# Performance work log

Measured on AMD Instinct MI355X. Metric: run time of the kernel, lower is better.

## Reference

```python
import jax, jax.numpy as jnp
import numpy as np

OBS_DIM = 256
ACTION_DIM = 4
NUM_OBJECTS = 16
HIDDEN = 512
BATCH = 4096
LN_EPS = 1e-5


def _uniform(key, shape, stdv):
    return jax.random.uniform(key, shape, jnp.float32, -stdv, stdv)


def setup_inputs() -> dict:
    key = jax.random.key(0)
    ks = jax.random.split(key, 8)
    node_in = OBS_DIM + ACTION_DIM
    s1 = 1.0 / np.sqrt(HIDDEN)
    s3 = 1.0 / np.sqrt(OBS_DIM)
    return {
        "states": jax.random.normal(ks[0], (BATCH, NUM_OBJECTS, OBS_DIM), jnp.float32),
        "action": jax.random.randint(ks[1], (BATCH,), 0, ACTION_DIM * NUM_OBJECTS, jnp.int64 if jax.config.jax_enable_x64 else jnp.int32),
        "W1": _uniform(ks[2], (node_in, HIDDEN), s1),
        "b1": _uniform(ks[3], (HIDDEN,), s1),
        "W2": _uniform(ks[4], (HIDDEN, HIDDEN), s1),
        "b2": _uniform(ks[5], (HIDDEN,), s1),
        "W3": _uniform(ks[6], (HIDDEN, OBS_DIM), s3),
        "b3": _uniform(ks[7], (OBS_DIM,), s3),
        "ln_g": jnp.ones((HIDDEN,), jnp.float32),
        "ln_b": jnp.zeros((HIDDEN,), jnp.float32),
    }


def _gc(x, W, b):
    # x: [B, O, d_in]. adj = block_diag(ones(O,O)/O) == per-graph mean pooling,
    # broadcast back to every node in the graph.
    s = jnp.einsum("bod,dh->boh", x, W)
    m = jnp.mean(s, axis=1, keepdims=True)  # [B, 1, h]
    return jnp.broadcast_to(m, s.shape) + b


def _layernorm(x, g, b):
    mu = jnp.mean(x, axis=-1, keepdims=True)
    var = jnp.mean(jnp.square(x - mu), axis=-1, keepdims=True)
    return (x - mu) * jax.lax.rsqrt(var + LN_EPS) * g + b


def reference(states, action, W1, b1, W2, b2, W3, b3, ln_g, ln_b):
    B, O, D = states.shape
    # one_hot(action, A*O).view(-1, A) == per-node one-hot slices
    a = jax.nn.one_hot(action, ACTION_DIM * O, dtype=states.dtype)
    a = a.reshape(B, O, ACTION_DIM)
    x = jnp.concatenate([states, a], axis=-1)  # [B, O, D+A]
    h = jax.nn.relu(_gc(x, W1, b1))
    h = jax.nn.relu(_layernorm(_gc(h, W2, b2), ln_g, ln_b))
    out = _gc(h, W3, b3)  # [B, O, obs_dim]
    return out
```

## Files before the change

kernel.cpp:

```cpp
#include <hip/hip_runtime.h>
#include <hip/hip_bf16.h>

#define BSZ   4096
#define NOBJ  16
#define DOBS  256
#define ADIM  4
#define HID   512
#define KP1   288

#define MB    16
#define NT    512
#define XP1   296
#define HP    520
#define TP    260

typedef unsigned short u16;
typedef __bf16 bf16x8 __attribute__((ext_vector_type(8)));
typedef float  f32x4  __attribute__((ext_vector_type(4)));
typedef unsigned short u16x8 __attribute__((ext_vector_type(8)));
typedef unsigned short u16x4 __attribute__((ext_vector_type(4)));

static __device__ __forceinline__ u16 f2bf(float f) {
    __hip_bfloat16 h = __float2bfloat16(f);
    return __builtin_bit_cast(u16, h);
}
static __device__ __forceinline__ bf16x8 ldg8(const u16* p) {
    return __builtin_bit_cast(bf16x8, *(const u16x8*)p);
}

__global__ __launch_bounds__(256) void prep_weights(
    const float* __restrict__ W1, const float* __restrict__ W2,
    const float* __restrict__ W3,
    u16* __restrict__ W1T, u16* __restrict__ W2T, u16* __restrict__ W3T) {
    int bid = blockIdx.x;
    const float* src; u16* dst; int Ksrc, H, Kp, tk, th;
    if (bid < 144)      { src = W1; dst = W1T; Ksrc = 260; H = 512; Kp = 288; tk = bid / 16;        th = bid % 16; }
    else if (bid < 400) { src = W2; dst = W2T; Ksrc = 512; H = 512; Kp = 512; tk = (bid-144) / 16;  th = (bid-144) % 16; }
    else                { src = W3; dst = W3T; Ksrc = 512; H = 256; Kp = 512; tk = (bid-400) / 8;   th = (bid-400) % 8; }

    __shared__ float tile[32][33];
    int tx = threadIdx.x & 31, ty = threadIdx.x >> 5;
    #pragma unroll
    for (int i = 0; i < 4; ++i) {
        int k = tk * 32 + ty + i * 8;
        int h = th * 32 + tx;
        tile[ty + i * 8][tx] = (k < Ksrc) ? src[(size_t)k * H + h] : 0.f;
    }
    __syncthreads();
    #pragma unroll
    for (int i = 0; i < 4; ++i) {
        int h = th * 32 + ty + i * 8;
        int k = tk * 32 + tx;
        dst[(size_t)h * Kp + k] = f2bf(tile[tx][ty + i * 8]);
    }
}

__global__ __launch_bounds__(NT) void fused_mlp(
    const float* __restrict__ states, const int* __restrict__ action,
    const u16* __restrict__ W1T, const float* __restrict__ b1,
    const u16* __restrict__ W2T, const float* __restrict__ b2,
    const u16* __restrict__ W3T, const float* __restrict__ b3,
    const float* __restrict__ lng, const float* __restrict__ lnb,
    float* __restrict__ out)
{
    __shared__ u16   xbar[MB][XP1];
    __shared__ u16   h1[MB][HP];
    __shared__ u16   h2[MB][HP];
    __shared__ float t3[MB][TP];
    __shared__ float red[2][8][MB];

    const int t  = threadIdx.x;
    const int w  = t >> 6;
    const int l  = t & 63;
    const int lr = l & 15;
    const int lg = l >> 4;
    const int b0 = blockIdx.x * MB;

    {
        const float4* sf4 = (const float4*)states;
        #pragma unroll
        for (int p = 0; p < 2; ++p) {
            int idx = p * NT + t;
            int r = idx >> 6, d4 = idx & 63;
            float sx = 0.f, sy = 0.f, sz = 0.f, sw = 0.f;
            const float4* rp = sf4 + (((size_t)(b0 + r) * NOBJ) << 6) + d4;
            #pragma unroll
            for (int o = 0; o < NOBJ; ++o) {
                float4 v = rp[o << 6];
                sx += v.x; sy += v.y; sz += v.z; sw += v.w;
            }
            u16x4 st = { f2bf(sx * (1.0f / NOBJ)), f2bf(sy * (1.0f / NOBJ)),
                         f2bf(sz * (1.0f / NOBJ)), f2bf(sw * (1.0f / NOBJ)) };
            *(u16x4*)&xbar[r][d4 * 4] = st;
        }
        if (t < MB) {
            int a = action[b0 + t] & 3;
            #pragma unroll
            for (int k = 0; k < KP1 - DOBS; ++k)
                xbar[t][DOBS + k] = f2bf(k == a ? (1.0f / NOBJ) : 0.0f);
        }
    }
    __syncthreads();

    {
        f32x4 acc[4] = {};
        #pragma unroll 3
        for (int ks = 0; ks < KP1 / 32; ++ks) {
            bf16x8 a = ldg8(&xbar[lr][ks * 32 + lg * 8]);
            #pragma unroll
            for (int nb = 0; nb < 4; ++nb) {
                int n = w * 64 + nb * 16 + lr;
                bf16x8 bv = ldg8(W1T + (size_t)n * KP1 + ks * 32 + lg * 8);
                acc[nb] = __builtin_amdgcn_mfma_f32_16x16x32_bf16(a, bv, acc[nb], 0, 0, 0);
            }
        }
        #pragma unroll
        for (int nb = 0; nb < 4; ++nb) {
            int n = w * 64 + nb * 16 + lr;
            float bias = b1[n];
            #pragma unroll
            for (int r = 0; r < 4; ++r)
                h1[lg * 4 + r][n] = f2bf(fmaxf(acc[nb][r] + bias, 0.f));
        }
    }
    __syncthreads();

    {
        f32x4 acc[4] = {};
        #pragma unroll 4
        for (int ks = 0; ks < HID / 32; ++ks) {
            bf16x8 a = ldg8(&h1[lr][ks * 32 + lg * 8]);
            #pragma unroll
            for (int nb = 0; nb < 4; ++nb) {
                int n = w * 64 + nb * 16 + lr;
                bf16x8 bv = ldg8(W2T + (size_t)n * HID + ks * 32 + lg * 8);
                acc[nb] = __builtin_amdgcn_mfma_f32_16x16x32_bf16(a, bv, acc[nb], 0, 0, 0);
            }
        }
        float s1[4] = {0.f, 0.f, 0.f, 0.f}, s2[4] = {0.f, 0.f, 0.f, 0.f};
        #pragma unroll
        for (int nb = 0; nb < 4; ++nb) {
            float bias = b2[w * 64 + nb * 16 + lr];
            #pragma unroll
            for (int r = 0; r < 4; ++r) {
                float v = acc[nb][r] + bias;
                acc[nb][r] = v;
                s1[r] += v;
                s2[r] += v * v;
            }
        }
        #pragma unroll
        for (int r = 0; r < 4; ++r) {
            #pragma unroll
            for (int m = 8; m; m >>= 1) {
                s1[r] += __shfl_xor(s1[r], m, 64);
                s2[r] += __shfl_xor(s2[r], m, 64);
            }
            if (lr == 0) {
                red[0][w][lg * 4 + r] = s1[r];
                red[1][w][lg * 4 + r] = s2[r];
            }
        }
        __syncthreads();
        float muv[4], rsv[4];
        #pragma unroll
        for (int r = 0; r < 4; ++r) {
            int m = lg * 4 + r;
            float S1 = 0.f, S2 = 0.f;
            #pragma unroll
            for (int ww = 0; ww < 8; ++ww) { S1 += red[0][ww][m]; S2 += red[1][ww][m]; }
            float mu = S1 * (1.0f / HID);
            float var = S2 * (1.0f / HID) - mu * mu;
            muv[r] = mu;
            rsv[r] = rsqrtf(var + 1e-5f);
        }
        #pragma unroll
        for (int nb = 0; nb < 4; ++nb) {
            int n = w * 64 + nb * 16 + lr;
            float g = lng[n], bb = lnb[n];
            #pragma unroll
            for (int r = 0; r < 4; ++r) {
                float y = (acc[nb][r] - muv[r]) * rsv[r] * g + bb;
                h2[lg * 4 + r][n] = f2bf(fmaxf(y, 0.f));
            }
        }
    }
    __syncthreads();

    {
        f32x4 acc[2] = {};
        #pragma unroll 4
        for (int ks = 0; ks < HID / 32; ++ks) {
            bf16x8 a = ldg8(&h2[lr][ks * 32 + lg * 8]);
            #pragma unroll
            for (int nb = 0; nb < 2; ++nb) {
                int n = w * 32 + nb * 16 + lr;
                bf16x8 bv = ldg8(W3T + (size_t)n * HID + ks * 32 + lg * 8);
                acc[nb] = __builtin_amdgcn_mfma_f32_16x16x32_bf16(a, bv, acc[nb], 0, 0, 0);
            }
        }
        #pragma unroll
        for (int nb = 0; nb < 2; ++nb) {
            int n = w * 32 + nb * 16 + lr;
            float bias = b3[n];
            #pragma unroll
            for (int r = 0; r < 4; ++r)
                t3[lg * 4 + r][n] = acc[nb][r] + bias;
        }
    }
    __syncthreads();

    {
        #pragma unroll 8
        for (int i = 0; i < 32; ++i) {
            int flat = i * NT + t;
            int d4 = flat & 63;
            int o  = (flat >> 6) & 15;
            int r  = flat >> 10;
            float4 v = *(const float4*)&t3[r][d4 * 4];
            *(float4*)(out + ((size_t)(b0 + r) * NOBJ + o) * DOBS + d4 * 4) = v;
        }
    }
}

extern "C" void kernel_launch(void* const* d_in, const int* in_sizes, int n_in,
                              void* d_out, int out_size, void* d_ws, size_t ws_size,
                              hipStream_t stream) {
    const float* states = (const float*)d_in[0];
    const int*   action = (const int*)d_in[1];
    const float* W1 = (const float*)d_in[2];
    const float* b1 = (const float*)d_in[3];
    const float* W2 = (const float*)d_in[4];
    const float* b2 = (const float*)d_in[5];
    const float* W3 = (const float*)d_in[6];
    const float* b3 = (const float*)d_in[7];
    const float* lng = (const float*)d_in[8];
    const float* lnb = (const float*)d_in[9];
    float* out = (float*)d_out;

    char* ws = (char*)d_ws;
    size_t off = 0;
    auto alloc = [&](size_t bytes) -> void* {
        void* p = ws + off;
        off = (off + bytes + 255) & ~(size_t)255;
        return p;
    };
    u16* W1T = (u16*)alloc((size_t)HID * KP1 * 2);
    u16* W2T = (u16*)alloc((size_t)HID * HID * 2);
    u16* W3T = (u16*)alloc((size_t)DOBS * HID * 2);

    prep_weights<<<528, 256, 0, stream>>>(W1, W2, W3, W1T, W2T, W3T);
    fused_mlp<<<BSZ / MB, NT, 0, stream>>>(states, action,
                                           W1T, b1, W2T, b2, W3T, b3,
                                           lng, lnb, out);
}
```

Measured before the change: 157.8 us.

## Split state mean-reduction into separate high-parallelism kernel before MLP

Moves the per-graph mean pooling of states and the one-hot action encoding out of the fused MLP kernel into a dedicated reduce kernel with 1024 blocks. The bf16 pooled features go through a global workspace buffer, and the MLP kernel then loads them into shared memory. The aim is to spread the 64 MB state read across many more blocks, since the fused kernel had only 256 blocks to hide that memory traffic. In exchange it adds a kernel launch and a small extra global round trip.

```diff
diff --git a/kernel.cpp b/kernel.cpp
--- a/kernel.cpp
+++ b/kernel.cpp
@@ -55,8 +55,36 @@
     }
 }
 
-__global__ __launch_bounds__(NT) void fused_mlp(
+__global__ __launch_bounds__(256) void reduce_states(
     const float* __restrict__ states, const int* __restrict__ action,
+    u16* __restrict__ xg) {
+    int t = threadIdx.x;
+    int r = blockIdx.x * 4 + (t >> 6);
+    int d4 = t & 63;
+    const float4* rp = (const float4*)states + (((size_t)r * NOBJ) << 6) + d4;
+    float sx = 0.f, sy = 0.f, sz = 0.f, sw = 0.f;
+    #pragma unroll
+    for (int o = 0; o < NOBJ; ++o) {
+        float4 v = rp[o << 6];
+        sx += v.x; sy += v.y; sz += v.z; sw += v.w;
+    }
+    u16x4 st = { f2bf(sx * (1.0f / NOBJ)), f2bf(sy * (1.0f / NOBJ)),
+                 f2bf(sz * (1.0f / NOBJ)), f2bf(sw * (1.0f / NOBJ)) };
+    *(u16x4*)(xg + (size_t)r * KP1 + d4 * 4) = st;
+    if (t < 32) {
+        int rl = t >> 3, c = t & 7;
+        int r2 = blockIdx.x * 4 + rl;
+        int a = action[r2] & 3;
+        u16x4 v = { (u16)0, (u16)0, (u16)0, (u16)0 };
+        #pragma unroll
+        for (int j = 0; j < 4; ++j)
+            if (c * 4 + j == a) v[j] = f2bf(1.0f / NOBJ);
+        *(u16x4*)(xg + (size_t)r2 * KP1 + DOBS + c * 4) = v;
+    }
+}
+
+__global__ __launch_bounds__(NT) void mlp(
+    const u16* __restrict__ xg,
     const u16* __restrict__ W1T, const float* __restrict__ b1,
     const u16* __restrict__ W2T, const float* __restrict__ b2,
     const u16* __restrict__ W3T, const float* __restrict__ b3,
@@ -77,27 +105,11 @@
     const int b0 = blockIdx.x * MB;
 
     {
-        const float4* sf4 = (const float4*)states;
-        #pragma unroll
-        for (int p = 0; p < 2; ++p) {
-            int idx = p * NT + t;
-            int r = idx >> 6, d4 = idx & 63;
-            float sx = 0.f, sy = 0.f, sz = 0.f, sw = 0.f;
-            const float4* rp = sf4 + (((size_t)(b0 + r) * NOBJ) << 6) + d4;
-            #pragma unroll
-            for (int o = 0; o < NOBJ; ++o) {
-                float4 v = rp[o << 6];
-                sx += v.x; sy += v.y; sz += v.z; sw += v.w;
-            }
-            u16x4 st = { f2bf(sx * (1.0f / NOBJ)), f2bf(sy * (1.0f / NOBJ)),
-                         f2bf(sz * (1.0f / NOBJ)), f2bf(sw * (1.0f / NOBJ)) };
-            *(u16x4*)&xbar[r][d4 * 4] = st;
-        }
-        if (t < MB) {
-            int a = action[b0 + t] & 3;
-            #pragma unroll
-            for (int k = 0; k < KP1 - DOBS; ++k)
-                xbar[t][DOBS + k] = f2bf(k == a ? (1.0f / NOBJ) : 0.0f);
+        const u16x4* src = (const u16x4*)(xg + (size_t)b0 * KP1);
+        #pragma unroll
+        for (int i = t; i < MB * (KP1 / 4); i += NT) {
+            int r = i / (KP1 / 4), c = i % (KP1 / 4);
+            *(u16x4*)&xbar[r][c * 4] = src[i];
         }
     }
     __syncthreads();
@@ -248,9 +260,10 @@
     u16* W1T = (u16*)alloc((size_t)HID * KP1 * 2);
     u16* W2T = (u16*)alloc((size_t)HID * HID * 2);
     u16* W3T = (u16*)alloc((size_t)DOBS * HID * 2);
+    u16* xg  = (u16*)alloc((size_t)BSZ * KP1 * 2);
 
     prep_weights<<<528, 256, 0, stream>>>(W1, W2, W3, W1T, W2T, W3T);
-    fused_mlp<<<BSZ / MB, NT, 0, stream>>>(states, action,
-                                           W1T, b1, W2T, b2, W3T, b3,
-                                           lng, lnb, out);
-}
+    reduce_states<<<BSZ / 4, 256, 0, stream>>>(states, action, xg);
+    mlp<<<BSZ / MB, NT, 0, stream>>>(xg, W1T, b1, W2T, b2, W3T, b3,
+                                     lng, lnb, out);
+}
```

New measurement: 162.1 us. 1.03x slower.
